# Kernel optimization log

Measured on AMD Instinct MI355X. Metric: run time of the kernel, lower is better.

The kernel has to match this reference:

```python
import jax, jax.numpy as jnp
import numpy as np

EMBED_DIM = 1024
NUM_HEADS = 16
HEAD_DIM = EMBED_DIM // NUM_HEADS
FF_DIM = 4096
B, T = 4, 1024


def setup_inputs() -> dict:
    key = jax.random.key(0)
    ks = jax.random.split(key, 13)
    E, F = EMBED_DIM, FF_DIM
    s_e = 1.0 / np.sqrt(E)
    s_f = 1.0 / np.sqrt(F)
    return {
        "x": jax.random.normal(ks[0], (B, T, E), dtype=jnp.float32),
        "ln1_w": jnp.ones((E,), jnp.float32),
        "ln1_b": jnp.zeros((E,), jnp.float32),
        "ln2_w": jnp.ones((E,), jnp.float32),
        "ln2_b": jnp.zeros((E,), jnp.float32),
        "qkv_w": jax.random.uniform(ks[1], (3 * E, E), jnp.float32, -s_e, s_e),
        "qkv_b": jax.random.uniform(ks[2], (3 * E,), jnp.float32, -s_e, s_e),
        "out_w": jax.random.uniform(ks[3], (E, E), jnp.float32, -s_e, s_e),
        "out_b": jax.random.uniform(ks[4], (E,), jnp.float32, -s_e, s_e),
        "fc1_w": jax.random.uniform(ks[5], (F, E), jnp.float32, -s_e, s_e),
        "fc1_b": jax.random.uniform(ks[6], (F,), jnp.float32, -s_e, s_e),
        "fc2_w": jax.random.uniform(ks[7], (E, F), jnp.float32, -s_f, s_f),
        "fc2_b": jax.random.uniform(ks[8], (E,), jnp.float32, -s_f, s_f),
    }


def _layer_norm(x, w, b, eps=1e-5):
    mu = jnp.mean(x, axis=-1, keepdims=True)
    var = jnp.mean(jnp.square(x - mu), axis=-1, keepdims=True)
    return (x - mu) * jax.lax.rsqrt(var + eps) * w + b


def reference(x, ln1_w, ln1_b, ln2_w, ln2_b, qkv_w, qkv_b, out_w, out_b,
              fc1_w, fc1_b, fc2_w, fc2_b):
    Bn, Tn, C = x.shape
    H, D = NUM_HEADS, HEAD_DIM

    # --- causal self-attention (pre-LN) ---
    h = _layer_norm(x, ln1_w, ln1_b)
    qkv = h @ qkv_w.T + qkv_b  # [B,T,3E]
    qkv = qkv.reshape(Bn, Tn, 3, H, D).transpose(2, 0, 3, 1, 4)  # [3,B,H,T,D]
    q, k, v = qkv[0], qkv[1], qkv[2]
    scores = jnp.einsum("bhtd,bhsd->bhts", q, k) / np.sqrt(D).astype(np.float32)
    causal = jnp.tril(jnp.ones((Tn, Tn), dtype=bool))
    scores = jnp.where(causal, scores, -jnp.inf)
    probs = jax.nn.softmax(scores, axis=-1)  # dropout is identity at eval
    attn = jnp.einsum("bhts,bhsd->bhtd", probs, v)
    attn = attn.transpose(0, 2, 1, 3).reshape(Bn, Tn, C)
    attn = attn @ out_w.T + out_b
    x = x + attn

    # --- GELU MLP (pre-LN) ---
    h = _layer_norm(x, ln2_w, ln2_b)
    h = jax.nn.gelu(h @ fc1_w.T + fc1_b, approximate=False)
    h = h @ fc2_w.T + fc2_b
    return x + h
```

## Files before the change

### kernel.cpp

```cpp
#include <hip/hip_runtime.h>

typedef float floatx4 __attribute__((ext_vector_type(4)));
typedef short shortx8 __attribute__((ext_vector_type(8)));

#define E_DIM 1024
#define F_DIM 4096
#define BATCH 4
#define SEQ 1024
#define NH 16
#define HD 64
#define MROWS (BATCH*SEQ)
#define QKV_N (3*E_DIM)

typedef const __attribute__((address_space(1))) unsigned int* gas_ptr;
typedef __attribute__((address_space(3))) unsigned int* las_ptr;

__device__ __forceinline__ unsigned short f2bf(float f) {
    union { float f; unsigned u; } un; un.f = f;
    unsigned u = un.u;
    u += 0x7fffu + ((u >> 16) & 1u);
    return (unsigned short)(u >> 16);
}

__device__ __forceinline__ float gelu_fast(float v) {
    float u = 0.7978845608f * (v + 0.044715f * v * v * v);
    float t = __builtin_exp2f(-2.885390082f * u);
    return v * __builtin_amdgcn_rcpf(1.0f + t);
}

__device__ __forceinline__ void xcd_remap(int& m_idx, int& n_idx) {
    int nt = gridDim.x;
    int mt_x = gridDim.y >> 3;
    int lin = blockIdx.y * nt + blockIdx.x;
    int xcd = lin & 7, loc = lin >> 3;
    int n = loc / mt_x;
    int m_local = loc - n * mt_x;
    m_idx = xcd * mt_x + m_local;
    n_idx = n;
}

#define S_QKV (3*E_DIM*E_DIM)
#define S_WO  (E_DIM*E_DIM)
#define S_W1  (F_DIM*E_DIM)
#define S_TOT (S_QKV + S_WO + 2*S_W1)
__global__ __launch_bounds__(256) void f2b_all(
        const float* __restrict__ qkv_w, const float* __restrict__ out_w,
        const float* __restrict__ fc1_w, const float* __restrict__ fc2_w,
        unsigned short* __restrict__ wq, unsigned short* __restrict__ wo,
        unsigned short* __restrict__ w1, unsigned short* __restrict__ w2) {
    long idx = ((long)blockIdx.x * 256 + threadIdx.x) * 4;
    const float* src; unsigned short* dst; long off;
    if (idx < S_QKV)                    { src = qkv_w; dst = wq; off = idx; }
    else if (idx < S_QKV + S_WO)        { src = out_w; dst = wo; off = idx - S_QKV; }
    else if (idx < S_QKV + S_WO + S_W1) { src = fc1_w; dst = w1; off = idx - S_QKV - S_WO; }
    else                                { src = fc2_w; dst = w2; off = idx - S_QKV - S_WO - S_W1; }
    float4 v = *(const float4*)&src[off];
    ushort4 o;
    o.x = f2bf(v.x); o.y = f2bf(v.y); o.z = f2bf(v.z); o.w = f2bf(v.w);
    *(ushort4*)&dst[off] = o;
}

__global__ __launch_bounds__(256) void ln_kernel(const float* __restrict__ x,
                                                 const float* __restrict__ w,
                                                 const float* __restrict__ b,
                                                 unsigned short* __restrict__ out) {
    int row = blockIdx.x;
    const float* xr = x + (size_t)row * E_DIM;
    float v[4];
    float s = 0.f, ss = 0.f;
    for (int i = 0; i < 4; ++i) {
        v[i] = xr[threadIdx.x + i * 256];
        s += v[i]; ss += v[i] * v[i];
    }
    for (int m = 32; m; m >>= 1) { s += __shfl_xor(s, m); ss += __shfl_xor(ss, m); }
    __shared__ float red[8];
    int wave = threadIdx.x >> 6;
    if ((threadIdx.x & 63) == 0) { red[wave] = s; red[wave + 4] = ss; }
    __syncthreads();
    s = red[0] + red[1] + red[2] + red[3];
    ss = red[4] + red[5] + red[6] + red[7];
    float mu = s * (1.0f / E_DIM);
    float var = ss * (1.0f / E_DIM) - mu * mu;
    float rs = rsqrtf(var + 1e-5f);
    for (int i = 0; i < 4; ++i) {
        int c = threadIdx.x + i * 256;
        out[(size_t)row * E_DIM + c] = f2bf((v[i] - mu) * rs * w[c] + b[c]);
    }
}

#define TM 128
#define TN 128
#define BK 64

template<int EPI>
__global__ __launch_bounds__(1024) void gemm_16w(
        const unsigned short* __restrict__ A, const unsigned short* __restrict__ Bw,
        const float* __restrict__ bias, const float* __restrict__ resid,
        float* __restrict__ Cf, unsigned short* __restrict__ Cb,
        int M, int N, int K) {
    __shared__ unsigned short sA[2][256 * BK];
    __shared__ unsigned short sB[2][256 * BK];
    int tid = threadIdx.x;
    int wave = tid >> 6, lane = tid & 63;
    int m_idx, n_idx; xcd_remap(m_idx, n_idx);
    int m0 = m_idx * 256, n0 = n_idx * 256;
    int wm = (wave >> 2) * 64, wn = (wave & 3) * 64;
    int l15 = lane & 15, quad = lane >> 4;

    int srow = tid >> 3;
    int scg  = (tid & 7) ^ (srow & 7);
    const unsigned short* Ag = A  + (size_t)(m0 + srow) * K + scg * 8;
    const unsigned short* Bg = Bw + (size_t)(n0 + srow) * K + scg * 8;

    floatx4 acc[4][4];
#pragma unroll
    for (int i = 0; i < 4; ++i)
#pragma unroll
        for (int j = 0; j < 4; ++j) acc[i][j] = (floatx4)0.f;

    auto stage = [&](int kt, int bsel) {
        int k0 = kt * BK;
#pragma unroll
        for (int p = 0; p < 2; ++p) {
            __builtin_amdgcn_global_load_lds((gas_ptr)(Ag + k0 + (size_t)p * 128 * K),
                (las_ptr)&sA[bsel][(p * 128 + wave * 8) * BK], 16, 0, 0);
            __builtin_amdgcn_global_load_lds((gas_ptr)(Bg + k0 + (size_t)p * 128 * K),
                (las_ptr)&sB[bsel][(p * 128 + wave * 8) * BK], 16, 0, 0);
        }
    };

    int T = K / BK;
    stage(0, 0);
    stage(1, 1);
    for (int i = 0; i < T; ++i) {
        if (i + 1 < T) { asm volatile("s_waitcnt vmcnt(4)" ::: "memory"); }
        else           { asm volatile("s_waitcnt vmcnt(0)" ::: "memory"); }
        __builtin_amdgcn_s_barrier();
        int bs = i & 1;
#pragma unroll
        for (int kk8 = 0; kk8 < 8; kk8 += 4) {
            shortx8 af[4], bfr[4];
#pragma unroll
            for (int ii = 0; ii < 4; ++ii) {
                int R = wm + ii * 16 + l15;
                int sc = (quad + kk8) ^ (R & 7);
                af[ii] = *(const shortx8*)&sA[bs][(R * 8 + sc) * 8];
            }
#pragma unroll
            for (int j = 0; j < 4; ++j) {
                int R = wn + j * 16 + l15;
                int sc = (quad + kk8) ^ (R & 7);
                bfr[j] = *(const shortx8*)&sB[bs][(R * 8 + sc) * 8];
            }
#pragma unroll
            for (int ii = 0; ii < 4; ++ii)
#pragma unroll
                for (int j = 0; j < 4; ++j)
                    acc[ii][j] = __builtin_amdgcn_mfma_f32_16x16x32_bf16(af[ii], bfr[j], acc[ii][j], 0, 0, 0);
        }
        __builtin_amdgcn_s_barrier();
        if (i + 2 < T) stage(i + 2, bs);
    }

#pragma unroll
    for (int i = 0; i < 4; ++i) {
        int row = m0 + wm + i * 16 + quad * 4;
#pragma unroll
        for (int j = 0; j < 4; ++j) {
            int col = n0 + wn + j * 16 + l15;
            float bs2 = bias[col];
#pragma unroll
            for (int r = 0; r < 4; ++r) {
                float v = acc[i][j][r] + bs2;
                int rr = row + r;
                if (EPI & 1) v = gelu_fast(v);
                if (EPI & 2) v += resid[(size_t)rr * N + col];
                if (EPI & 4) Cf[(size_t)rr * N + col] = v;
                if (EPI & 8) Cb[(size_t)rr * N + col] = f2bf(v);
            }
        }
    }
}

template<int EPI>
__global__ __launch_bounds__(512) void gemm_n64(
        const unsigned short* __restrict__ A, const unsigned short* __restrict__ Bw,
        const float* __restrict__ bias, const float* __restrict__ resid,
        float* __restrict__ Cf, unsigned short* __restrict__ Cb,
        int M, int N, int K) {
    __shared__ unsigned short sA[2][TM * BK];
    __shared__ unsigned short sB[2][64 * BK];
    int tid = threadIdx.x;
    int wave = tid >> 6, lane = tid & 63;
    int m_idx, n_idx;
    xcd_remap(m_idx, n_idx);
    int n0 = n_idx * 64, m0 = m_idx * TM;
    int wm = (wave & 3) * 32, wn = (wave >> 2) * 32;
    int l15 = lane & 15, quad = lane >> 4;

    int srow = wave * 8 + (lane >> 3);
    int scg  = (lane & 7) ^ (srow & 7);
    const unsigned short* Ag = A  + (size_t)(m0 + srow) * K + scg * 8;
    const unsigned short* Bg = Bw + (size_t)(n0 + srow) * K + scg * 8;

    floatx4 acc[2][2];
#pragma unroll
    for (int i = 0; i < 2; ++i)
#pragma unroll
        for (int j = 0; j < 2; ++j) acc[i][j] = (floatx4)0.f;

    auto stage = [&](int kt, int bsel) {
        int k0 = kt * BK;
#pragma unroll
        for (int p = 0; p < 2; ++p)
            __builtin_amdgcn_global_load_lds((gas_ptr)(Ag + k0 + (size_t)p * 64 * K),
                (las_ptr)&sA[bsel][(p * 64 + wave * 8) * BK], 16, 0, 0);
        __builtin_amdgcn_global_load_lds((gas_ptr)(Bg + k0),
            (las_ptr)&sB[bsel][(wave * 8) * BK], 16, 0, 0);
    };

    int T = K / BK;
    stage(0, 0);
    stage(1, 1);
    for (int i = 0; i < T; ++i) {
        if (i + 1 < T) { asm volatile("s_waitcnt vmcnt(3)" ::: "memory"); }
        else           { asm volatile("s_waitcnt vmcnt(0)" ::: "memory"); }
        __builtin_amdgcn_s_barrier();
        int bs = i & 1;
#pragma unroll
        for (int kk8 = 0; kk8 < 8; kk8 += 4) {
            shortx8 af[2], bfr[2];
#pragma unroll
            for (int ii = 0; ii < 2; ++ii) {
                int R = wm + ii * 16 + l15;
                int sc = (quad + kk8) ^ (R & 7);
                af[ii] = *(const shortx8*)&sA[bs][(R * 8 + sc) * 8];
            }
#pragma unroll
            for (int j = 0; j < 2; ++j) {
                int R = wn + j * 16 + l15;
                int sc = (quad + kk8) ^ (R & 7);
                bfr[j] = *(const shortx8*)&sB[bs][(R * 8 + sc) * 8];
            }
#pragma unroll
            for (int ii = 0; ii < 2; ++ii)
#pragma unroll
                for (int j = 0; j < 2; ++j)
                    acc[ii][j] = __builtin_amdgcn_mfma_f32_16x16x32_bf16(af[ii], bfr[j], acc[ii][j], 0, 0, 0);
        }
        __builtin_amdgcn_s_barrier();
        if (i + 2 < T) stage(i + 2, bs);
    }

#pragma unroll
    for (int i = 0; i < 2; ++i) {
        int row = m0 + wm + i * 16 + quad * 4;
#pragma unroll
        for (int j = 0; j < 2; ++j) {
            int col = n0 + wn + j * 16 + l15;
            float bs2 = bias[col];
#pragma unroll
            for (int r = 0; r < 4; ++r) {
                float v = acc[i][j][r] + bs2;
                int rr = row + r;
                if (EPI & 1) v = gelu_fast(v);
                if (EPI & 2) v += resid[(size_t)rr * N + col];
                if (EPI & 4) Cf[(size_t)rr * N + col] = v;
                if (EPI & 8) Cb[(size_t)rr * N + col] = f2bf(v);
            }
        }
    }
}

__global__ __launch_bounds__(256) void vtrans_kernel(const unsigned short* __restrict__ qkv,
                                                     unsigned short* __restrict__ vT) {
    __shared__ unsigned short tile[64 * 72];
    int tid = threadIdx.x;
    int bh = blockIdx.y, b = bh >> 4, h = bh & 15;
    int t0 = blockIdx.x * 64;
    const unsigned short* vsrc = qkv + (size_t)b * SEQ * QKV_N + 2 * E_DIM + h * HD;
#pragma unroll
    for (int p = 0; p < 2; ++p) {
        int idx = p * 256 + tid;
        int row = idx >> 3, col = (idx & 7) * 8;
        *(shortx8*)&tile[row * 72 + col] =
            *(const shortx8*)&vsrc[(size_t)(t0 + row) * QKV_N + col];
    }
    __syncthreads();
    int d = tid >> 2, tch = (tid & 3) * 16;
    unsigned short* dst = vT + (size_t)bh * HD * SEQ + (size_t)d * SEQ + t0 + tch;
    shortx8 a0, a1;
#pragma unroll
    for (int j = 0; j < 8; ++j) a0[j] = (short)tile[(tch + j) * 72 + d];
#pragma unroll
    for (int j = 0; j < 8; ++j) a1[j] = (short)tile[(tch + 8 + j) * 72 + d];
    *(shortx8*)&dst[0] = a0;
    *(shortx8*)&dst[8] = a1;
}

__global__ __launch_bounds__(256) void attn_kernel(
        const unsigned short* __restrict__ qkv, const unsigned short* __restrict__ vT,
        unsigned short* __restrict__ out) {
    __shared__ unsigned short kt[2][64 * 64];
    __shared__ unsigned short vt[2][64 * 64];
    __shared__ unsigned short ps[4][16 * 64];
    int tid = threadIdx.x;
    int wave = tid >> 6, lane = tid & 63, l15 = lane & 15, quad = lane >> 4;
    int bh = blockIdx.y, b = bh >> 4, h = bh & 15;
    const unsigned short* qbase = qkv + (size_t)b * SEQ * QKV_N + h * HD;
    const unsigned short* kbase = qbase + E_DIM;
    const unsigned short* vtb = vT + (size_t)bh * HD * SEQ;

    int srl = lane >> 3;
    int scg = (lane & 7) ^ srl;

    const float scale = 0.125f * 1.44269504f;

    auto stage = [&](int t, int bsel) {
        int s0 = t * 64;
#pragma unroll
        for (int p = 0; p < 2; ++p) {
            int rbase = p * 32 + wave * 8;
            __builtin_amdgcn_global_load_lds(
                (gas_ptr)&kbase[(size_t)(s0 + rbase + srl) * QKV_N + scg * 8],
                (las_ptr)&kt[bsel][rbase * 64], 16, 0, 0);
            __builtin_amdgcn_global_load_lds(
                (gas_ptr)&vtb[(size_t)(rbase + srl) * SEQ + s0 + scg * 8],
                (las_ptr)&vt[bsel][rbase * 64], 16, 0, 0);
        }
    };

    for (int pass = 0; pass < 2; ++pass) {
        int qt = (pass == 0) ? blockIdx.x : (15 - blockIdx.x);
        int q0 = qt * 64;
        int qrow = q0 + wave * 16;

        shortx8 qa0 = *(const shortx8*)&qbase[(size_t)(qrow + l15) * QKV_N + quad * 8];
        shortx8 qa1 = *(const shortx8*)&qbase[(size_t)(qrow + l15) * QKV_N + 32 + quad * 8];

        floatx4 o[4];
        for (int d = 0; d < 4; ++d) o[d] = (floatx4)0.f;
        float mrun[4], lrun[4];
        for (int r = 0; r < 4; ++r) { mrun[r] = -1e30f; lrun[r] = 0.f; }

        int ntile = qt + 1;
        __syncthreads();
        stage(0, 0);
        for (int t = 0; t < ntile; ++t) {
            asm volatile("s_waitcnt vmcnt(0)" ::: "memory");
            __builtin_amdgcn_s_barrier();
            if (t + 1 < ntile) stage(t + 1, (t + 1) & 1);
            int bsel = t & 1;
            int s0 = t * 64;

            floatx4 sfr[4];
#pragma unroll
            for (int ct = 0; ct < 4; ++ct) {
                int R = ct * 16 + l15;
                int sc0 = quad ^ (R & 7), sc1 = (4 + quad) ^ (R & 7);
                shortx8 kb0 = *(const shortx8*)&kt[bsel][(R * 8 + sc0) * 8];
                shortx8 kb1 = *(const shortx8*)&kt[bsel][(R * 8 + sc1) * 8];
                floatx4 s4 = (floatx4)0.f;
                s4 = __builtin_amdgcn_mfma_f32_16x16x32_bf16(qa0, kb0, s4, 0, 0, 0);
                s4 = __builtin_amdgcn_mfma_f32_16x16x32_bf16(qa1, kb1, s4, 0, 0, 0);
                sfr[ct] = s4;
            }

            bool masked = (t == ntile - 1);
#pragma unroll
            for (int r = 0; r < 4; ++r) {
                int qg = qrow + quad * 4 + r;
                float sv[4];
                float mx = mrun[r];
#pragma unroll
                for (int ct = 0; ct < 4; ++ct) {
                    float v = sfr[ct][r] * scale;
                    if (masked && (s0 + ct * 16 + l15 > qg)) v = -1e30f;
                    sv[ct] = v;
                    mx = fmaxf(mx, v);
                }
                for (int mm = 8; mm; mm >>= 1) mx = fmaxf(mx, __shfl_xor(mx, mm));
                float alpha = exp2f(mrun[r] - mx);
                mrun[r] = mx;
                float sum = 0.f;
                float pv[4];
#pragma unroll
                for (int ct = 0; ct < 4; ++ct) { pv[ct] = exp2f(sv[ct] - mx); sum += pv[ct]; }
                for (int mm = 8; mm; mm >>= 1) sum += __shfl_xor(sum, mm);
                lrun[r] = lrun[r] * alpha + sum;
#pragma unroll
                for (int d = 0; d < 4; ++d) o[d][r] *= alpha;
                int row = quad * 4 + r;
#pragma unroll
                for (int ct = 0; ct < 4; ++ct) {
                    int g = ct * 2 + (l15 >> 3);
                    int sc = g ^ (row & 7);
                    ps[wave][row * 64 + sc * 8 + (l15 & 7)] = f2bf(pv[ct]);
                }
            }
            shortx8 pa0, pa1;
            {
                int sc0 = quad ^ (l15 & 7), sc1 = (4 + quad) ^ (l15 & 7);
                pa0 = *(const shortx8*)&ps[wave][(l15 * 8 + sc0) * 8];
                pa1 = *(const shortx8*)&ps[wave][(l15 * 8 + sc1) * 8];
            }
#pragma unroll
            for (int d = 0; d < 4; ++d) {
                int R = d * 16 + l15;
                int sc0 = quad ^ (R & 7), sc1 = (4 + quad) ^ (R & 7);
                shortx8 vb0 = *(const shortx8*)&vt[bsel][(R * 8 + sc0) * 8];
                shortx8 vb1 = *(const shortx8*)&vt[bsel][(R * 8 + sc1) * 8];
                o[d] = __builtin_amdgcn_mfma_f32_16x16x32_bf16(pa0, vb0, o[d], 0, 0, 0);
                o[d] = __builtin_amdgcn_mfma_f32_16x16x32_bf16(pa1, vb1, o[d], 0, 0, 0);
            }
        }

#pragma unroll
        for (int r = 0; r < 4; ++r) {
            float inv = 1.0f / lrun[r];
            int m = (b << 10) + qrow + quad * 4 + r;
#pragma unroll
            for (int d = 0; d < 4; ++d)
                out[(size_t)m * E_DIM + h * HD + d * 16 + l15] = f2bf(o[d][r] * inv);
        }
    }
}

extern "C" void kernel_launch(void* const* d_in, const int* in_sizes, int n_in,
                              void* d_out, int out_size, void* d_ws, size_t ws_size,
                              hipStream_t stream) {
    const float* x     = (const float*)d_in[0];
    const float* ln1_w = (const float*)d_in[1];
    const float* ln1_b = (const float*)d_in[2];
    const float* ln2_w = (const float*)d_in[3];
    const float* ln2_b = (const float*)d_in[4];
    const float* qkv_w = (const float*)d_in[5];
    const float* qkv_b = (const float*)d_in[6];
    const float* out_w = (const float*)d_in[7];
    const float* out_b = (const float*)d_in[8];
    const float* fc1_w = (const float*)d_in[9];
    const float* fc1_b = (const float*)d_in[10];
    const float* fc2_w = (const float*)d_in[11];
    const float* fc2_b = (const float*)d_in[12];

    char* ws = (char*)d_ws;
    size_t off = 0;
    auto alloc = [&](size_t bytes) { char* p = ws + off; off += bytes; return p; };
    unsigned short* wq   = (unsigned short*)alloc((size_t)3 * E_DIM * E_DIM * 2);
    unsigned short* wo   = (unsigned short*)alloc((size_t)E_DIM * E_DIM * 2);
    unsigned short* w1   = (unsigned short*)alloc((size_t)F_DIM * E_DIM * 2);
    unsigned short* w2   = (unsigned short*)alloc((size_t)E_DIM * F_DIM * 2);
    unsigned short* h1   = (unsigned short*)alloc((size_t)MROWS * E_DIM * 2);
    unsigned short* qkvb = (unsigned short*)alloc((size_t)MROWS * QKV_N * 2);
    unsigned short* vT   = (unsigned short*)alloc((size_t)BATCH * NH * HD * SEQ * 2);
    unsigned short* attn = (unsigned short*)alloc((size_t)MROWS * E_DIM * 2);
    float*          x1   = (float*)alloc((size_t)MROWS * E_DIM * 4);
    unsigned short* h2   = (unsigned short*)alloc((size_t)MROWS * E_DIM * 2);
    unsigned short* g    = (unsigned short*)alloc((size_t)MROWS * F_DIM * 2);

    f2b_all<<<S_TOT / 4 / 256, 256, 0, stream>>>(qkv_w, out_w, fc1_w, fc2_w, wq, wo, w1, w2);

    ln_kernel<<<MROWS, 256, 0, stream>>>(x, ln1_w, ln1_b, h1);
    gemm_16w<8><<<dim3(QKV_N / 256, MROWS / 256), 1024, 0, stream>>>(
        h1, wq, qkv_b, nullptr, nullptr, qkvb, MROWS, QKV_N, E_DIM);
    vtrans_kernel<<<dim3(SEQ / 64, BATCH * NH), 256, 0, stream>>>(qkvb, vT);
    attn_kernel<<<dim3(8, BATCH * NH), 256, 0, stream>>>(qkvb, vT, attn);
    gemm_n64<2 | 4><<<dim3(E_DIM / 64, MROWS / TM), 512, 0, stream>>>(
        attn, wo, out_b, x, x1, nullptr, MROWS, E_DIM, E_DIM);
    ln_kernel<<<MROWS, 256, 0, stream>>>(x1, ln2_w, ln2_b, h2);
    gemm_16w<1 | 8><<<dim3(F_DIM / 256, MROWS / 256), 1024, 0, stream>>>(
        h2, w1, fc1_b, nullptr, nullptr, g, MROWS, F_DIM, E_DIM);
    gemm_n64<2 | 4><<<dim3(E_DIM / 64, MROWS / TM), 512, 0, stream>>>(
        g, w2, fc2_b, x1, (float*)d_out, nullptr, MROWS, E_DIM, F_DIM);
}
```

Baseline: 315.2 us.

## Replace N64 GEMM with 128x128 intra-block split-K GEMM for out-proj and fc2

The 128x64-tile, 512-thread GEMM used for the output projection and fc2 is replaced by a 1024-thread kernel with 128x128 tiles and BK=128. Its 16 waves split the K slice four ways, and partial accumulators are reduced through shared memory before the bias/residual epilogue. The goal is more reuse per loaded tile and more MFMA work per barrier. The cost is fewer blocks (256 instead of 512, so less parallelism on 256 CUs), 128KB of LDS, and an extra reduction phase.

```diff
diff --git a/kernel.cpp b/kernel.cpp
--- a/kernel.cpp
+++ b/kernel.cpp
@@ -88,8 +88,6 @@
     }
 }
 
-#define TM 128
-#define TN 128
 #define BK 64
 
 template<int EPI>
@@ -183,90 +181,121 @@
 }
 
 template<int EPI>
-__global__ __launch_bounds__(512) void gemm_n64(
+__global__ __launch_bounds__(1024) void gemm_ksp(
         const unsigned short* __restrict__ A, const unsigned short* __restrict__ Bw,
         const float* __restrict__ bias, const float* __restrict__ resid,
         float* __restrict__ Cf, unsigned short* __restrict__ Cb,
         int M, int N, int K) {
-    __shared__ unsigned short sA[2][TM * BK];
-    __shared__ unsigned short sB[2][64 * BK];
+    __shared__ unsigned short smem[2][2][128 * 128];
     int tid = threadIdx.x;
     int wave = tid >> 6, lane = tid & 63;
-    int m_idx, n_idx;
-    xcd_remap(m_idx, n_idx);
-    int n0 = n_idx * 64, m0 = m_idx * TM;
-    int wm = (wave & 3) * 32, wn = (wave >> 2) * 32;
+    int m_idx, n_idx; xcd_remap(m_idx, n_idx);
+    int m0 = m_idx * 128, n0 = n_idx * 128;
+    int kq = wave & 3, mi = (wave >> 2) & 1, ni = wave >> 3;
     int l15 = lane & 15, quad = lane >> 4;
-
-    int srow = wave * 8 + (lane >> 3);
-    int scg  = (lane & 7) ^ (srow & 7);
-    const unsigned short* Ag = A  + (size_t)(m0 + srow) * K + scg * 8;
-    const unsigned short* Bg = Bw + (size_t)(n0 + srow) * K + scg * 8;
-
-    floatx4 acc[2][2];
-#pragma unroll
-    for (int i = 0; i < 2; ++i)
-#pragma unroll
-        for (int j = 0; j < 2; ++j) acc[i][j] = (floatx4)0.f;
-
-    auto stage = [&](int kt, int bsel) {
-        int k0 = kt * BK;
-#pragma unroll
-        for (int p = 0; p < 2; ++p)
-            __builtin_amdgcn_global_load_lds((gas_ptr)(Ag + k0 + (size_t)p * 64 * K),
-                (las_ptr)&sA[bsel][(p * 64 + wave * 8) * BK], 16, 0, 0);
-        __builtin_amdgcn_global_load_lds((gas_ptr)(Bg + k0),
-            (las_ptr)&sB[bsel][(wave * 8) * BK], 16, 0, 0);
+    int kh = kq >> 1, cb = (kq & 1) * 4;
+
+    int lu = wave * 8 + (lane >> 3);
+
+    floatx4 acc[4][4];
+#pragma unroll
+    for (int i = 0; i < 4; ++i)
+#pragma unroll
+        for (int j = 0; j < 4; ++j) acc[i][j] = (floatx4)0.f;
+
+    auto stage = [&](int kt, int b) {
+#pragma unroll
+        for (int p = 0; p < 2; ++p) {
+            int u = p * 128 + lu;
+            int row = u >> 1, uh = u & 1;
+            int scg = (lane & 7) ^ (row & 7);
+            __builtin_amdgcn_global_load_lds(
+                (gas_ptr)(A + (size_t)(m0 + row) * K + kt * 128 + uh * 64 + scg * 8),
+                (las_ptr)&smem[b][0][(p * 128 + wave * 8) * 64], 16, 0, 0);
+        }
+#pragma unroll
+        for (int p = 0; p < 2; ++p) {
+            int u = p * 128 + lu;
+            int row = u >> 1, uh = u & 1;
+            int scg = (lane & 7) ^ (row & 7);
+            __builtin_amdgcn_global_load_lds(
+                (gas_ptr)(Bw + (size_t)(n0 + row) * K + kt * 128 + uh * 64 + scg * 8),
+                (las_ptr)&smem[b][1][(p * 128 + wave * 8) * 64], 16, 0, 0);
+        }
     };
 
-    int T = K / BK;
+    int T = K / 128;
     stage(0, 0);
     stage(1, 1);
     for (int i = 0; i < T; ++i) {
-        if (i + 1 < T) { asm volatile("s_waitcnt vmcnt(3)" ::: "memory"); }
+        if (i + 1 < T) { asm volatile("s_waitcnt vmcnt(4)" ::: "memory"); }
         else           { asm volatile("s_waitcnt vmcnt(0)" ::: "memory"); }
         __builtin_amdgcn_s_barrier();
         int bs = i & 1;
-#pragma unroll
-        for (int kk8 = 0; kk8 < 8; kk8 += 4) {
-            shortx8 af[2], bfr[2];
-#pragma unroll
-            for (int ii = 0; ii < 2; ++ii) {
-                int R = wm + ii * 16 + l15;
-                int sc = (quad + kk8) ^ (R & 7);
-                af[ii] = *(const shortx8*)&sA[bs][(R * 8 + sc) * 8];
-            }
-#pragma unroll
-            for (int j = 0; j < 2; ++j) {
-                int R = wn + j * 16 + l15;
-                int sc = (quad + kk8) ^ (R & 7);
-                bfr[j] = *(const shortx8*)&sB[bs][(R * 8 + sc) * 8];
-            }
-#pragma unroll
-            for (int ii = 0; ii < 2; ++ii)
-#pragma unroll
-                for (int j = 0; j < 2; ++j)
-                    acc[ii][j] = __builtin_amdgcn_mfma_f32_16x16x32_bf16(af[ii], bfr[j], acc[ii][j], 0, 0, 0);
-        }
+        shortx8 af[4], bfr[4];
+#pragma unroll
+        for (int ii = 0; ii < 4; ++ii) {
+            int R = mi * 64 + ii * 16 + l15;
+            int sc = (cb + quad) ^ (R & 7);
+            af[ii] = *(const shortx8*)&smem[bs][0][((R * 2 + kh) * 8 + sc) * 8];
+        }
+#pragma unroll
+        for (int j = 0; j < 4; ++j) {
+            int R = ni * 64 + j * 16 + l15;
+            int sc = (cb + quad) ^ (R & 7);
+            bfr[j] = *(const shortx8*)&smem[bs][1][((R * 2 + kh) * 8 + sc) * 8];
+        }
+#pragma unroll
+        for (int ii = 0; ii < 4; ++ii)
+#pragma unroll
+            for (int j = 0; j < 4; ++j)
+                acc[ii][j] = __builtin_amdgcn_mfma_f32_16x16x32_bf16(af[ii], bfr[j], acc[ii][j], 0, 0, 0);
         __builtin_amdgcn_s_barrier();
         if (i + 2 < T) stage(i + 2, bs);
     }
 
-#pragma unroll
-    for (int i = 0; i < 2; ++i) {
-        int row = m0 + wm + i * 16 + quad * 4;
-#pragma unroll
-        for (int j = 0; j < 2; ++j) {
-            int col = n0 + wn + j * 16 + l15;
-            float bs2 = bias[col];
-#pragma unroll
-            for (int r = 0; r < 4; ++r) {
-                float v = acc[i][j][r] + bs2;
-                int rr = row + r;
-                if (EPI & 1) v = gelu_fast(v);
-                if (EPI & 2) v += resid[(size_t)rr * N + col];
-                if (EPI & 4) Cf[(size_t)rr * N + col] = v;
-                if (EPI & 8) Cb[(size_t)rr * N + col] = f2bf(v);
+    float* red = (float*)&smem[0][0][0];
+    int base = (mi * 2 + ni) * 2;
+    auto wracc = [&](int rid) {
+#pragma unroll
+        for (int i2 = 0; i2 < 4; ++i2)
+#pragma unroll
+            for (int j2 = 0; j2 < 4; ++j2)
+                *(floatx4*)&red[(size_t)rid * 4096 + ((i2 * 4 + j2) * 64 + lane) * 4] = acc[i2][j2];
+    };
+    auto rdacc = [&](int rid) {
+#pragma unroll
+        for (int i2 = 0; i2 < 4; ++i2)
+#pragma unroll
+            for (int j2 = 0; j2 < 4; ++j2) {
+                floatx4 v = *(const floatx4*)&red[(size_t)rid * 4096 + ((i2 * 4 + j2) * 64 + lane) * 4];
+                acc[i2][j2] += v;
+            }
+    };
+    if (kq >= 2) wracc(base + (kq - 2));
+    __syncthreads();
+    if (kq < 2) rdacc(base + kq);
+    __syncthreads();
+    if (kq == 1) wracc(base);
+    __syncthreads();
+    if (kq == 0) {
+        rdacc(base);
+#pragma unroll
+        for (int i = 0; i < 4; ++i) {
+            int row = m0 + mi * 64 + i * 16 + quad * 4;
+#pragma unroll
+            for (int j = 0; j < 4; ++j) {
+                int col = n0 + ni * 64 + j * 16 + l15;
+                float bs2 = bias[col];
+#pragma unroll
+                for (int r = 0; r < 4; ++r) {
+                    float v = acc[i][j][r] + bs2;
+                    int rr = row + r;
+                    if (EPI & 1) v = gelu_fast(v);
+                    if (EPI & 2) v += resid[(size_t)rr * N + col];
+                    if (EPI & 4) Cf[(size_t)rr * N + col] = v;
+                    if (EPI & 8) Cb[(size_t)rr * N + col] = f2bf(v);
+                }
             }
         }
     }
@@ -465,11 +494,11 @@
         h1, wq, qkv_b, nullptr, nullptr, qkvb, MROWS, QKV_N, E_DIM);
     vtrans_kernel<<<dim3(SEQ / 64, BATCH * NH), 256, 0, stream>>>(qkvb, vT);
     attn_kernel<<<dim3(8, BATCH * NH), 256, 0, stream>>>(qkvb, vT, attn);
-    gemm_n64<2 | 4><<<dim3(E_DIM / 64, MROWS / TM), 512, 0, stream>>>(
+    gemm_ksp<2 | 4><<<dim3(E_DIM / 128, MROWS / 128), 1024, 0, stream>>>(
         attn, wo, out_b, x, x1, nullptr, MROWS, E_DIM, E_DIM);
     ln_kernel<<<MROWS, 256, 0, stream>>>(x1, ln2_w, ln2_b, h2);
     gemm_16w<1 | 8><<<dim3(F_DIM / 256, MROWS / 256), 1024, 0, stream>>>(
         h2, w1, fc1_b, nullptr, nullptr, g, MROWS, F_DIM, E_DIM);
-    gemm_n64<2 | 4><<<dim3(E_DIM / 64, MROWS / TM), 512, 0, stream>>>(
+    gemm_ksp<2 | 4><<<dim3(E_DIM / 128, MROWS / 128), 1024, 0, stream>>>(
         g, w2, fc2_b, x1, (float*)d_out, nullptr, MROWS, E_DIM, F_DIM);
 }
```

Result: no change. 313.7 us (-0.5%).
